# Performance work log

Hardware: AMD Instinct MI355X
Metric: run time of the kernel (lower is better)

Reference implementation:

```python
import jax, jax.numpy as jnp
import numpy as np

N = 50000          # num nodes
E = 800000         # num edges (before self loops)
F_IN = 128         # input node features
HID = 64           # hidden_dim from source
HEADS = 4
NUM_CLASSES = 5
NEG_SLOPE = 0.2    # PyG GATConv default negative_slope


def setup_inputs() -> dict:
    key = jax.random.key(0)
    ks = jax.random.split(key, 14)
    def gl(k, shape, fan):
        return jax.random.normal(k, shape, jnp.float32) * (1.0 / np.sqrt(fan))
    x = jax.random.normal(ks[0], (N, F_IN), jnp.float32)
    edge_index = jax.random.randint(ks[1], (2, E), 0, N, dtype=jnp.int32)
    # layer 1: in=128, heads=4, out=64, concat
    W1 = gl(ks[2], (F_IN, HEADS * HID), F_IN)
    a_src1 = gl(ks[3], (HEADS, HID), HID)
    a_dst1 = gl(ks[4], (HEADS, HID), HID)
    b1 = jax.random.normal(ks[5], (HEADS * HID,), jnp.float32) * 0.01
    # layer 2: in=256, heads=4, out=64, concat
    W2 = gl(ks[6], (HEADS * HID, HEADS * HID), HEADS * HID)
    a_src2 = gl(ks[7], (HEADS, HID), HID)
    a_dst2 = gl(ks[8], (HEADS, HID), HID)
    b2 = jax.random.normal(ks[9], (HEADS * HID,), jnp.float32) * 0.01
    # layer 3: in=256, heads=1, out=5, concat (heads=1)
    W3 = gl(ks[10], (HEADS * HID, 1 * NUM_CLASSES), HEADS * HID)
    a_src3 = gl(ks[11], (1, NUM_CLASSES), NUM_CLASSES)
    a_dst3 = gl(ks[12], (1, NUM_CLASSES), NUM_CLASSES)
    b3 = jax.random.normal(ks[13], (NUM_CLASSES,), jnp.float32) * 0.01
    return {"x": x, "edge_index": edge_index,
            "W1": W1, "a_src1": a_src1, "a_dst1": a_dst1, "b1": b1,
            "W2": W2, "a_src2": a_src2, "a_dst2": a_dst2, "b2": b2,
            "W3": W3, "a_src3": a_src3, "a_dst3": a_dst3, "b3": b3}


def gat_conv(x, src, dst, W, a_src, a_dst, b, heads, out_ch):
    """PyG-style GATConv (concat=True, eval mode, self-loops already in src/dst)."""
    n = x.shape[0]
    h = (x @ W).reshape(n, heads, out_ch)              # [N,H,C]
    al_s = jnp.sum(h * a_src, axis=-1)                 # [N,H]
    al_d = jnp.sum(h * a_dst, axis=-1)                 # [N,H]
    # per-edge unnormalized attention
    e = jax.nn.leaky_relu(al_s[src] + al_d[dst], NEG_SLOPE)   # [E,H]
    # segment softmax over incoming edges of each destination node
    m = jax.ops.segment_max(e, dst, num_segments=n)    # [N,H]
    e = jnp.exp(e - m[dst])
    s = jax.ops.segment_sum(e, dst, num_segments=n)    # [N,H]
    alpha = e / (s[dst] + 1e-16)                       # [E,H]
    # gather-weight-scatter aggregation
    out = jax.ops.segment_sum(h[src] * alpha[..., None], dst, num_segments=n)  # [N,H,C]
    return out.reshape(n, heads * out_ch) + b


def reference(x, edge_index, W1, a_src1, a_dst1, b1, W2, a_src2, a_dst2, b2,
              W3, a_src3, a_dst3, b3):
    n = x.shape[0]
    # PyG GATConv adds self-loops by default
    loops = jnp.arange(n, dtype=edge_index.dtype)
    src = jnp.concatenate([edge_index[0], loops])
    dst = jnp.concatenate([edge_index[1], loops])
    h = jax.nn.relu(gat_conv(x, src, dst, W1, a_src1, a_dst1, b1, HEADS, HID))
    h = jax.nn.relu(gat_conv(h, src, dst, W2, a_src2, a_dst2, b2, HEADS, HID))
    out = gat_conv(h, src, dst, W3, a_src3, a_dst3, b3, 1, NUM_CLASSES)
    return out
```

## Files before the change

kernel.cpp:

```cpp
#include <hip/hip_runtime.h>
#include <hip/hip_bf16.h>
#include <cstddef>


typedef _Float16 h4 __attribute__((ext_vector_type(4)));

#define TILE_BM 128
#define TILE_BN 128
#define TILE_KB 16
#define ECAP 96


__global__ void zero_i32(int* __restrict__ p, int n) {
  int i = blockIdx.x * 256 + threadIdx.x;
  if (i < n) p[i] = 0;
}

__global__ void edge_histogram(const int* __restrict__ ei, int E, int nnodes,
                               int* __restrict__ counts) {
  int e = blockIdx.x * 256 + threadIdx.x;
  int tot = E + nnodes;
  if (e >= tot) return;
  int dst = (e < E) ? ei[E + e] : (e - E);
  atomicAdd(&counts[dst], 1);
}

__global__ void scan_block(const int* __restrict__ in, int* __restrict__ out,
                           int* __restrict__ sums, int n) {
  __shared__ int tmp[256];
  int i = blockIdx.x * 256 + threadIdx.x;
  int v = (i < n) ? in[i] : 0;
  tmp[threadIdx.x] = v;
  __syncthreads();
  for (int off = 1; off < 256; off <<= 1) {
    int t = (threadIdx.x >= off) ? tmp[threadIdx.x - off] : 0;
    __syncthreads();
    tmp[threadIdx.x] += t;
    __syncthreads();
  }
  if (i < n) out[i] = tmp[threadIdx.x] - v;
  if (sums && threadIdx.x == 255) sums[blockIdx.x] = tmp[255];
}

__global__ void add_offsets(int* __restrict__ row_ptr, const int* __restrict__ offs,
                            int* __restrict__ nextp, int n, int total) {
  int i = blockIdx.x * 256 + threadIdx.x;
  if (i < n) {
    int v = row_ptr[i] + offs[blockIdx.x];
    row_ptr[i] = v;
    nextp[i] = v;
  }
  if (i == 0) row_ptr[n] = total;
}

__global__ void edge_scatter(const int* __restrict__ ei, int E, int nnodes,
                             int* __restrict__ nextp, int* __restrict__ col_idx) {
  int e = blockIdx.x * 256 + threadIdx.x;
  int tot = E + nnodes;
  if (e >= tot) return;
  int src = (e < E) ? ei[e] : (e - E);
  int dst = (e < E) ? ei[E + e] : (e - E);
  int pos = atomicAdd(&nextp[dst], 1);
  col_idx[pos] = src;
}


__global__ __launch_bounds__(256) void gemm_f32_h16(const float* __restrict__ A,
                                                    const float* __restrict__ B,
                                                    _Float16* __restrict__ C16,
                                                    int M, int N, int K) {
  __shared__ float As[TILE_KB][TILE_BM + 4];
  __shared__ float Bs[TILE_KB][TILE_BN];
  int t = threadIdx.x;
  int m0 = blockIdx.x * TILE_BM;
  int n0 = blockIdx.y * TILE_BN;
  int tx = t & 15, ty = t >> 4;

  float c[2][2][4][4];
#pragma unroll
  for (int a = 0; a < 2; ++a)
#pragma unroll
    for (int b = 0; b < 2; ++b)
#pragma unroll
      for (int i = 0; i < 4; ++i)
#pragma unroll
        for (int j = 0; j < 4; ++j) c[a][b][i][j] = 0.f;

  for (int k0 = 0; k0 < K; k0 += TILE_KB) {
#pragma unroll
    for (int r = 0; r < 2; ++r) {
      int idx = t + r * 256;
      int row = idx >> 2;
      int quad = idx & 3;
      float4 v = {0.f, 0.f, 0.f, 0.f};
      int gr = m0 + row;
      if (gr < M) v = *(const float4*)&A[(size_t)gr * K + k0 + quad * 4];
      As[quad * 4 + 0][row] = v.x;
      As[quad * 4 + 1][row] = v.y;
      As[quad * 4 + 2][row] = v.z;
      As[quad * 4 + 3][row] = v.w;
    }
#pragma unroll
    for (int r = 0; r < 2; ++r) {
      int idx = t + r * 256;
      int krow = idx >> 5;
      int q = idx & 31;
      float4 v = *(const float4*)&B[(size_t)(k0 + krow) * N + n0 + q * 4];
      *(float4*)&Bs[krow][q * 4] = v;
    }
    __syncthreads();
#pragma unroll
    for (int k = 0; k < TILE_KB; ++k) {
      float4 a0 = *(const float4*)&As[k][ty * 4];
      float4 a1 = *(const float4*)&As[k][64 + ty * 4];
      float4 b0 = *(const float4*)&Bs[k][tx * 4];
      float4 b1 = *(const float4*)&Bs[k][64 + tx * 4];
      float av[2][4] = {{a0.x, a0.y, a0.z, a0.w}, {a1.x, a1.y, a1.z, a1.w}};
      float bv[2][4] = {{b0.x, b0.y, b0.z, b0.w}, {b1.x, b1.y, b1.z, b1.w}};
#pragma unroll
      for (int ih = 0; ih < 2; ++ih)
#pragma unroll
        for (int jh = 0; jh < 2; ++jh)
#pragma unroll
          for (int i = 0; i < 4; ++i)
#pragma unroll
            for (int j = 0; j < 4; ++j)
              c[ih][jh][i][j] += av[ih][i] * bv[jh][j];
    }
    __syncthreads();
  }
#pragma unroll
  for (int ih = 0; ih < 2; ++ih)
#pragma unroll
    for (int i = 0; i < 4; ++i) {
      int gr = m0 + ih * 64 + ty * 4 + i;
      if (gr >= M) continue;
#pragma unroll
      for (int jh = 0; jh < 2; ++jh) {
        h4 v = {(_Float16)c[ih][jh][i][0], (_Float16)c[ih][jh][i][1],
                (_Float16)c[ih][jh][i][2], (_Float16)c[ih][jh][i][3]};
        *(h4*)&C16[(size_t)gr * N + n0 + jh * 64 + tx * 4] = v;
      }
    }
}


__global__ __launch_bounds__(256) void compute_al(const _Float16* __restrict__ h,
                                                  const float* __restrict__ a_src,
                                                  const float* __restrict__ a_dst,
                                                  float* __restrict__ al_s,
                                                  float* __restrict__ al_d,
                                                  int nnodes) {
  int n = blockIdx.x * 4 + (threadIdx.x >> 6);
  if (n >= nnodes) return;
  int l = threadIdx.x & 63;
  h4 hv4 = *(const h4*)&h[(size_t)n * 256 + l * 4];
  float4 as4 = *(const float4*)&a_src[l * 4];
  float4 ad4 = *(const float4*)&a_dst[l * 4];
  float hx = (float)hv4[0], hy = (float)hv4[1], hz = (float)hv4[2],
        hw = (float)hv4[3];
  float ps = hx * as4.x + hy * as4.y + hz * as4.z + hw * as4.w;
  float pd = hx * ad4.x + hy * ad4.y + hz * ad4.z + hw * ad4.w;
#pragma unroll
  for (int off = 1; off < 16; off <<= 1) {
    ps += __shfl_xor(ps, off);
    pd += __shfl_xor(pd, off);
  }
  if ((l & 15) == 0) {
    al_s[n * 4 + (l >> 4)] = ps;
    al_d[n * 4 + (l >> 4)] = pd;
  }
}


template <bool RELU>
__global__ __launch_bounds__(256) void gat_aggregate(
    const _Float16* __restrict__ h, const float* __restrict__ al_s,
    const float* __restrict__ al_d, const int* __restrict__ row_ptr,
    const int* __restrict__ col_idx, const float* __restrict__ bias,
    float* __restrict__ out, int nnodes) {
  __shared__ float e_lds[4][ECAP * 4];
  int wv = threadIdx.x >> 6;
  int n = blockIdx.x * 4 + wv;
  if (n >= nnodes) return;
  int l = threadIdx.x & 63;
  int hd = l >> 4;
  int sub = l & 15;
  int beg = row_ptr[n], end = row_ptr[n + 1];
  int deg = end - beg;
  float ad = al_d[n * 4 + hd];

  float m = -3.0e38f;
  for (int j0 = 0; j0 < deg; j0 += 16) {
    int j = j0 + sub;
    float e = -3.0e38f;
    if (j < deg) {
      int src = col_idx[beg + j];
      e = al_s[src * 4 + hd] + ad;
      e = fmaxf(e, 0.2f * e);
      if (j < ECAP) e_lds[wv][j * 4 + hd] = e;
    }
    m = fmaxf(m, e);
  }
#pragma unroll
  for (int off = 1; off < 16; off <<= 1) m = fmaxf(m, __shfl_xor(m, off));
  __syncthreads();

  float s = 0.f;
  float4 acc = {0.f, 0.f, 0.f, 0.f};
  int jcap = deg < ECAP ? deg : ECAP;
  int j = 0;
  for (; j + 8 <= jcap; j += 8) {
    int si[8];
    h4 hv[8];
    float p[8];
#pragma unroll
    for (int u = 0; u < 8; ++u) si[u] = col_idx[beg + j + u];
#pragma unroll
    for (int u = 0; u < 8; ++u)
      hv[u] = *(const h4*)&h[(size_t)si[u] * 256 + l * 4];
#pragma unroll
    for (int u = 0; u < 8; ++u) p[u] = __expf(e_lds[wv][(j + u) * 4 + hd] - m);
#pragma unroll
    for (int u = 0; u < 8; ++u) {
      s += p[u];
      acc.x += p[u] * (float)hv[u][0];
      acc.y += p[u] * (float)hv[u][1];
      acc.z += p[u] * (float)hv[u][2];
      acc.w += p[u] * (float)hv[u][3];
    }
  }
  for (; j < deg; ++j) {
    int src = col_idx[beg + j];
    float e;
    if (j < ECAP) {
      e = e_lds[wv][j * 4 + hd];
    } else {
      e = al_s[src * 4 + hd] + ad;
      e = fmaxf(e, 0.2f * e);
    }
    float p = __expf(e - m);
    s += p;
    h4 hv = *(const h4*)&h[(size_t)src * 256 + l * 4];
    acc.x += p * (float)hv[0];
    acc.y += p * (float)hv[1];
    acc.z += p * (float)hv[2];
    acc.w += p * (float)hv[3];
  }
  float inv = 1.f / (s + 1e-16f);
  float4 bv = *(const float4*)&bias[l * 4];
  float4 o = {acc.x * inv + bv.x, acc.y * inv + bv.y, acc.z * inv + bv.z,
              acc.w * inv + bv.w};
  if (RELU) {
    o.x = fmaxf(o.x, 0.f);
    o.y = fmaxf(o.y, 0.f);
    o.z = fmaxf(o.z, 0.f);
    o.w = fmaxf(o.w, 0.f);
  }
  *(float4*)&out[(size_t)n * 256 + l * 4] = o;
}


__global__ __launch_bounds__(256) void gemm3_al(const float* __restrict__ Hin,
                                                const float* __restrict__ W3,
                                                const float* __restrict__ a_src3,
                                                const float* __restrict__ a_dst3,
                                                float* __restrict__ h3,
                                                float* __restrict__ al_s,
                                                float* __restrict__ al_d,
                                                int nnodes) {
  int n = blockIdx.x * 4 + (threadIdx.x >> 6);
  if (n >= nnodes) return;
  int l = threadIdx.x & 63;
  float4 hv = *(const float4*)&Hin[(size_t)n * 256 + l * 4];
  float acc[5];
#pragma unroll
  for (int cc = 0; cc < 5; ++cc) {
    acc[cc] = hv.x * W3[(l * 4 + 0) * 5 + cc] + hv.y * W3[(l * 4 + 1) * 5 + cc] +
              hv.z * W3[(l * 4 + 2) * 5 + cc] + hv.w * W3[(l * 4 + 3) * 5 + cc];
  }
#pragma unroll
  for (int cc = 0; cc < 5; ++cc)
#pragma unroll
    for (int off = 32; off; off >>= 1) acc[cc] += __shfl_xor(acc[cc], off);
  if (l == 0) {
    float as = 0.f, adv = 0.f;
#pragma unroll
    for (int cc = 0; cc < 5; ++cc) {
      h3[(size_t)n * 5 + cc] = acc[cc];
      as += acc[cc] * a_src3[cc];
      adv += acc[cc] * a_dst3[cc];
    }
    al_s[n] = as;
    al_d[n] = adv;
  }
}


__global__ __launch_bounds__(256) void gat_aggregate3(
    const float* __restrict__ h3, const float* __restrict__ al_s,
    const float* __restrict__ al_d, const int* __restrict__ row_ptr,
    const int* __restrict__ col_idx, const float* __restrict__ b3,
    float* __restrict__ out, int nnodes) {
  __shared__ float e_lds[4][ECAP];
  int wv = threadIdx.x >> 6;
  int n = blockIdx.x * 4 + wv;
  if (n >= nnodes) return;
  int l = threadIdx.x & 63;
  int beg = row_ptr[n], end = row_ptr[n + 1];
  int deg = end - beg;
  float ad = al_d[n];

  float m = -3.0e38f;
  for (int j0 = 0; j0 < deg; j0 += 64) {
    int j = j0 + l;
    float e = -3.0e38f;
    if (j < deg) {
      int src = col_idx[beg + j];
      e = al_s[src] + ad;
      e = fmaxf(e, 0.2f * e);
      if (j < ECAP) e_lds[wv][j] = e;
    }
    m = fmaxf(m, e);
  }
#pragma unroll
  for (int off = 1; off < 64; off <<= 1) m = fmaxf(m, __shfl_xor(m, off));

  float sp = 0.f;
  for (int j = l; j < deg; j += 64) {
    float e;
    if (j < ECAP) {
      e = e_lds[wv][j];
    } else {
      int src = col_idx[beg + j];
      e = al_s[src] + ad;
      e = fmaxf(e, 0.2f * e);
    }
    sp += __expf(e - m);
  }
#pragma unroll
  for (int off = 1; off < 64; off <<= 1) sp += __shfl_xor(sp, off);
  float s = sp;

  float acc = 0.f;
  if (l < 5) {
    for (int j = 0; j < deg; ++j) {
      float e;
      if (j < ECAP) {
        e = e_lds[wv][j];
      } else {
        int src0 = col_idx[beg + j];
        e = al_s[src0] + ad;
        e = fmaxf(e, 0.2f * e);
      }
      float p = __expf(e - m);
      int src = col_idx[beg + j];
      acc += p * h3[(size_t)src * 5 + l];
    }
    out[(size_t)n * 5 + l] = acc / (s + 1e-16f) + b3[l];
  }
}


extern "C" void kernel_launch(void* const* d_in, const int* in_sizes, int n_in,
                              void* d_out, int out_size, void* d_ws, size_t ws_size,
                              hipStream_t stream) {
  const float* x = (const float*)d_in[0];
  const int* ei = (const int*)d_in[1];
  const float* W1 = (const float*)d_in[2];
  const float* as1 = (const float*)d_in[3];
  const float* ad1 = (const float*)d_in[4];
  const float* b1 = (const float*)d_in[5];
  const float* W2 = (const float*)d_in[6];
  const float* as2 = (const float*)d_in[7];
  const float* ad2 = (const float*)d_in[8];
  const float* b2 = (const float*)d_in[9];
  const float* W3 = (const float*)d_in[10];
  const float* as3 = (const float*)d_in[11];
  const float* ad3 = (const float*)d_in[12];
  const float* b3 = (const float*)d_in[13];

  int N = in_sizes[0] / 128;
  int E = in_sizes[1] / 2;
  int tot = E + N;

  char* w = (char*)d_ws;
  size_t off = 0;
  auto alloc = [&](size_t bytes) -> void* {
    void* p = w + off;
    off += (bytes + 255) & ~(size_t)255;
    return p;
  };
  _Float16* h16 = (_Float16*)alloc((size_t)N * 256 * 2);
  float* bufB = (float*)alloc((size_t)N * 256 * 4);
  float* bufC = (float*)alloc((size_t)N * 256 * 4);
  float* h3 = (float*)alloc((size_t)N * 5 * 4);
  float* alS = (float*)alloc((size_t)N * 4 * 4);
  float* alD = (float*)alloc((size_t)N * 4 * 4);
  int* row_ptr = (int*)alloc(((size_t)N + 1) * 4);
  int* nextp = (int*)alloc((size_t)N * 4);
  int* bsums = (int*)alloc(256 * 4);
  int* col_idx = (int*)alloc((size_t)tot * 4);
  (void)ws_size;

  int nbN = (N + 255) / 256;
  int nbE = (tot + 255) / 256;
  int nb4 = (N + 3) / 4;

  zero_i32<<<nbN, 256, 0, stream>>>(nextp, N);
  edge_histogram<<<nbE, 256, 0, stream>>>(ei, E, N, nextp);
  scan_block<<<nbN, 256, 0, stream>>>(nextp, row_ptr, bsums, N);
  scan_block<<<1, 256, 0, stream>>>(bsums, bsums, nullptr, nbN);
  add_offsets<<<nbN, 256, 0, stream>>>(row_ptr, bsums, nextp, N, tot);
  edge_scatter<<<nbE, 256, 0, stream>>>(ei, E, N, nextp, col_idx);

  dim3 g1((N + TILE_BM - 1) / TILE_BM, 256 / TILE_BN);

  gemm_f32_h16<<<g1, 256, 0, stream>>>(x, W1, h16, N, 256, 128);
  compute_al<<<nb4, 256, 0, stream>>>(h16, as1, ad1, alS, alD, N);
  gat_aggregate<true><<<nb4, 256, 0, stream>>>(h16, alS, alD, row_ptr, col_idx,
                                               b1, bufB, N);
  gemm_f32_h16<<<g1, 256, 0, stream>>>(bufB, W2, h16, N, 256, 256);
  compute_al<<<nb4, 256, 0, stream>>>(h16, as2, ad2, alS, alD, N);
  gat_aggregate<true><<<nb4, 256, 0, stream>>>(h16, alS, alD, row_ptr, col_idx,
                                               b2, bufC, N);
  gemm3_al<<<nb4, 256, 0, stream>>>(bufC, W3, as3, ad3, h3, alS, alD, N);
  gat_aggregate3<<<nb4, 256, 0, stream>>>(h3, alS, alD, row_ptr, col_idx, b3,
                                          (float*)d_out, N);
}
```

Measured before the change: 571.8 us.

## Fuse attention-logit computation into GEMM epilogue and prefetch tiles via registers

Replaces the separate compute_al kernel by computing per-head source/destination attention logits in the GEMM epilogue with a 16-lane shuffle reduction, avoiding a re-read of the fp16 features and one launch per layer. The GEMM K-tile grows to 32 and global loads for the next tile are staged in registers while the current tile is computed. Logits now come from fp32 accumulators rather than fp16-rounded values, and register pressure rises.

```diff
diff --git a/kernel.cpp b/kernel.cpp
--- a/kernel.cpp
+++ b/kernel.cpp
@@ -5,9 +5,6 @@
 
 typedef _Float16 h4 __attribute__((ext_vector_type(4)));
 
-#define TILE_BM 128
-#define TILE_BN 128
-#define TILE_KB 16
 #define ECAP 96
 
 
@@ -65,17 +62,47 @@
 }
 
 
-__global__ __launch_bounds__(256) void gemm_f32_h16(const float* __restrict__ A,
-                                                    const float* __restrict__ B,
-                                                    _Float16* __restrict__ C16,
-                                                    int M, int N, int K) {
-  __shared__ float As[TILE_KB][TILE_BM + 4];
-  __shared__ float Bs[TILE_KB][TILE_BN];
+#define LOAD_TILE(k0)                                                        \
+  do {                                                                       \
+    _Pragma("unroll") for (int r = 0; r < 4; ++r) {                          \
+      int f = t + r * 256;                                                   \
+      int row = f >> 3, kq = f & 7;                                          \
+      int gr = m0 + row;                                                     \
+      ra[r] = (gr < M) ? *(const float4*)&A[(size_t)gr * K + (k0) + kq * 4]  \
+                       : make_float4(0.f, 0.f, 0.f, 0.f);                    \
+      int kr = f >> 5, cq = f & 31;                                          \
+      rb[r] = *(const float4*)&B[(size_t)((k0) + kr) * 256 + n0 + cq * 4];   \
+    }                                                                        \
+  } while (0)
+
+#define WRITE_TILE()                                                         \
+  do {                                                                       \
+    _Pragma("unroll") for (int r = 0; r < 4; ++r) {                          \
+      int f = t + r * 256;                                                   \
+      int row = f >> 3, kq = f & 7;                                          \
+      As[kq * 4 + 0][row] = ra[r].x;                                         \
+      As[kq * 4 + 1][row] = ra[r].y;                                         \
+      As[kq * 4 + 2][row] = ra[r].z;                                         \
+      As[kq * 4 + 3][row] = ra[r].w;                                         \
+      int kr = f >> 5, cq = f & 31;                                          \
+      *(float4*)&Bs[kr][cq * 4] = rb[r];                                     \
+    }                                                                        \
+  } while (0)
+
+__global__ __launch_bounds__(256) void gemm_al(
+    const float* __restrict__ A, const float* __restrict__ B,
+    _Float16* __restrict__ C16, const float* __restrict__ a_src,
+    const float* __restrict__ a_dst, float* __restrict__ alS,
+    float* __restrict__ alD, int M, int K) {
+  __shared__ float As[32][128 + 4];
+  __shared__ float Bs[32][128];
   int t = threadIdx.x;
-  int m0 = blockIdx.x * TILE_BM;
-  int n0 = blockIdx.y * TILE_BN;
+  int m0 = blockIdx.x * 128;
+  int by = blockIdx.y;
+  int n0 = by * 128;
   int tx = t & 15, ty = t >> 4;
 
+  float4 ra[4], rb[4];
   float c[2][2][4][4];
 #pragma unroll
   for (int a = 0; a < 2; ++a)
@@ -86,31 +113,14 @@
 #pragma unroll
         for (int j = 0; j < 4; ++j) c[a][b][i][j] = 0.f;
 
-  for (int k0 = 0; k0 < K; k0 += TILE_KB) {
-#pragma unroll
-    for (int r = 0; r < 2; ++r) {
-      int idx = t + r * 256;
-      int row = idx >> 2;
-      int quad = idx & 3;
-      float4 v = {0.f, 0.f, 0.f, 0.f};
-      int gr = m0 + row;
-      if (gr < M) v = *(const float4*)&A[(size_t)gr * K + k0 + quad * 4];
-      As[quad * 4 + 0][row] = v.x;
-      As[quad * 4 + 1][row] = v.y;
-      As[quad * 4 + 2][row] = v.z;
-      As[quad * 4 + 3][row] = v.w;
-    }
-#pragma unroll
-    for (int r = 0; r < 2; ++r) {
-      int idx = t + r * 256;
-      int krow = idx >> 5;
-      int q = idx & 31;
-      float4 v = *(const float4*)&B[(size_t)(k0 + krow) * N + n0 + q * 4];
-      *(float4*)&Bs[krow][q * 4] = v;
-    }
+  int ntiles = K >> 5;
+  LOAD_TILE(0);
+  WRITE_TILE();
+  for (int tt = 0; tt < ntiles; ++tt) {
     __syncthreads();
-#pragma unroll
-    for (int k = 0; k < TILE_KB; ++k) {
+    if (tt + 1 < ntiles) LOAD_TILE((tt + 1) * 32);
+#pragma unroll
+    for (int k = 0; k < 32; ++k) {
       float4 a0 = *(const float4*)&As[k][ty * 4];
       float4 a1 = *(const float4*)&As[k][64 + ty * 4];
       float4 b0 = *(const float4*)&Bs[k][tx * 4];
@@ -128,48 +138,46 @@
               c[ih][jh][i][j] += av[ih][i] * bv[jh][j];
     }
     __syncthreads();
-  }
+    if (tt + 1 < ntiles) WRITE_TILE();
+  }
+
+  float4 asv0 = *(const float4*)&a_src[(by * 2 + 0) * 64 + tx * 4];
+  float4 asv1 = *(const float4*)&a_src[(by * 2 + 1) * 64 + tx * 4];
+  float4 adv0 = *(const float4*)&a_dst[(by * 2 + 0) * 64 + tx * 4];
+  float4 adv1 = *(const float4*)&a_dst[(by * 2 + 1) * 64 + tx * 4];
 #pragma unroll
   for (int ih = 0; ih < 2; ++ih)
 #pragma unroll
     for (int i = 0; i < 4; ++i) {
       int gr = m0 + ih * 64 + ty * 4 + i;
-      if (gr >= M) continue;
-#pragma unroll
-      for (int jh = 0; jh < 2; ++jh) {
-        h4 v = {(_Float16)c[ih][jh][i][0], (_Float16)c[ih][jh][i][1],
-                (_Float16)c[ih][jh][i][2], (_Float16)c[ih][jh][i][3]};
-        *(h4*)&C16[(size_t)gr * N + n0 + jh * 64 + tx * 4] = v;
+      float* c0 = c[ih][0][i];
+      float* c1 = c[ih][1][i];
+      float ps0 = c0[0] * asv0.x + c0[1] * asv0.y + c0[2] * asv0.z + c0[3] * asv0.w;
+      float pd0 = c0[0] * adv0.x + c0[1] * adv0.y + c0[2] * adv0.z + c0[3] * adv0.w;
+      float ps1 = c1[0] * asv1.x + c1[1] * asv1.y + c1[2] * asv1.z + c1[3] * asv1.w;
+      float pd1 = c1[0] * adv1.x + c1[1] * adv1.y + c1[2] * adv1.z + c1[3] * adv1.w;
+#pragma unroll
+      for (int off = 1; off < 16; off <<= 1) {
+        ps0 += __shfl_xor(ps0, off);
+        pd0 += __shfl_xor(pd0, off);
+        ps1 += __shfl_xor(ps1, off);
+        pd1 += __shfl_xor(pd1, off);
       }
-    }
-}
-
-
-__global__ __launch_bounds__(256) void compute_al(const _Float16* __restrict__ h,
-                                                  const float* __restrict__ a_src,
-                                                  const float* __restrict__ a_dst,
-                                                  float* __restrict__ al_s,
-                                                  float* __restrict__ al_d,
-                                                  int nnodes) {
-  int n = blockIdx.x * 4 + (threadIdx.x >> 6);
-  if (n >= nnodes) return;
-  int l = threadIdx.x & 63;
-  h4 hv4 = *(const h4*)&h[(size_t)n * 256 + l * 4];
-  float4 as4 = *(const float4*)&a_src[l * 4];
-  float4 ad4 = *(const float4*)&a_dst[l * 4];
-  float hx = (float)hv4[0], hy = (float)hv4[1], hz = (float)hv4[2],
-        hw = (float)hv4[3];
-  float ps = hx * as4.x + hy * as4.y + hz * as4.z + hw * as4.w;
-  float pd = hx * ad4.x + hy * ad4.y + hz * ad4.z + hw * ad4.w;
-#pragma unroll
-  for (int off = 1; off < 16; off <<= 1) {
-    ps += __shfl_xor(ps, off);
-    pd += __shfl_xor(pd, off);
-  }
-  if ((l & 15) == 0) {
-    al_s[n * 4 + (l >> 4)] = ps;
-    al_d[n * 4 + (l >> 4)] = pd;
-  }
+      if (gr < M) {
+        h4 v0 = {(_Float16)c0[0], (_Float16)c0[1], (_Float16)c0[2],
+                 (_Float16)c0[3]};
+        h4 v1 = {(_Float16)c1[0], (_Float16)c1[1], (_Float16)c1[2],
+                 (_Float16)c1[3]};
+        *(h4*)&C16[(size_t)gr * 256 + n0 + tx * 4] = v0;
+        *(h4*)&C16[(size_t)gr * 256 + n0 + 64 + tx * 4] = v1;
+        if (tx == 0) {
+          alS[gr * 4 + by * 2 + 0] = ps0;
+          alS[gr * 4 + by * 2 + 1] = ps1;
+          alD[gr * 4 + by * 2 + 0] = pd0;
+          alD[gr * 4 + by * 2 + 1] = pd1;
+        }
+      }
+    }
 }
 
 
@@ -414,14 +422,12 @@
   add_offsets<<<nbN, 256, 0, stream>>>(row_ptr, bsums, nextp, N, tot);
   edge_scatter<<<nbE, 256, 0, stream>>>(ei, E, N, nextp, col_idx);
 
-  dim3 g1((N + TILE_BM - 1) / TILE_BM, 256 / TILE_BN);
-
-  gemm_f32_h16<<<g1, 256, 0, stream>>>(x, W1, h16, N, 256, 128);
-  compute_al<<<nb4, 256, 0, stream>>>(h16, as1, ad1, alS, alD, N);
+  dim3 g1((N + 127) / 128, 2);
+
+  gemm_al<<<g1, 256, 0, stream>>>(x, W1, h16, as1, ad1, alS, alD, N, 128);
   gat_aggregate<true><<<nb4, 256, 0, stream>>>(h16, alS, alD, row_ptr, col_idx,
                                                b1, bufB, N);
-  gemm_f32_h16<<<g1, 256, 0, stream>>>(bufB, W2, h16, N, 256, 256);
-  compute_al<<<nb4, 256, 0, stream>>>(h16, as2, ad2, alS, alD, N);
+  gemm_al<<<g1, 256, 0, stream>>>(bufB, W2, h16, as2, ad2, alS, alD, N, 256);
   gat_aggregate<true><<<nb4, 256, 0, stream>>>(h16, alS, alD, row_ptr, col_idx,
                                                b2, bufC, N);
   gemm3_al<<<nb4, 256, 0, stream>>>(bufC, W3, as3, ad3, h3, alS, alD, N);
```

New measurement: 1.238 ms. +116.6%, slower.
